# Performance work log

Measured on AMD Instinct MI355X. Metric: run time of the kernel, lower is better.

The kernel has to match this reference:

```python
import jax, jax.numpy as jnp
import numpy as np

N = 200_000          # active voxels
CIN, COUT = 64, 128  # in_filters, out_filters
GRID = (32, 480, 480)  # sparse spatial shape (D, H, W)
NEG_SLOPE = 0.01     # nn.LeakyReLU default
EPS = 1e-5           # BatchNorm1d default


def _build_nbrs():
    """Build rulebook-style neighbor tables for the two submanifold kernels.

    Returns nbr31 [9, N] for kernel (3,1,3) and nbr13 [9, N] for kernel (1,3,3).
    Entry == N means 'no active neighbor' (maps to a zero pad row).
    """
    rng = np.random.default_rng(0)
    prod = GRID[0] * GRID[1] * GRID[2]
    lin = rng.choice(prod, size=N, replace=False)
    z, y, x = np.unravel_index(lin, GRID)
    lut = np.full(prod, N, dtype=np.int64)
    lut[lin] = np.arange(N)

    def nbrs(offsets):
        out = np.full((len(offsets), N), N, dtype=np.int32)
        for k, (dz, dy, dx) in enumerate(offsets):
            zz, yy, xx = z + dz, y + dy, x + dx
            valid = ((zz >= 0) & (zz < GRID[0]) & (yy >= 0) & (yy < GRID[1])
                     & (xx >= 0) & (xx < GRID[2]))
            l2 = (zz * GRID[1] + yy) * GRID[2] + xx
            out[k, valid] = lut[l2[valid]].astype(np.int32)
        return out

    off31 = [(dz, 0, dx) for dz in (-1, 0, 1) for dx in (-1, 0, 1)]  # (3,1,3)
    off13 = [(0, dy, dx) for dy in (-1, 0, 1) for dx in (-1, 0, 1)]  # (1,3,3)
    return nbrs(off31), nbrs(off13)


def setup_inputs() -> dict:
    key = jax.random.key(0)
    ks = jax.random.split(key, 5)
    nbr31, nbr13 = _build_nbrs()
    s_in = (2.0 / (9 * CIN)) ** 0.5
    s_out = (2.0 / (9 * COUT)) ** 0.5
    ones = jnp.ones((COUT,), jnp.float32)
    zeros = jnp.zeros((COUT,), jnp.float32)
    return {
        "feats": jax.random.normal(ks[0], (N, CIN), jnp.float32),
        "W1": jax.random.normal(ks[1], (9, CIN, COUT), jnp.float32) * s_in,
        "W1_2": jax.random.normal(ks[2], (9, COUT, COUT), jnp.float32) * s_out,
        "W2": jax.random.normal(ks[3], (9, CIN, COUT), jnp.float32) * s_in,
        "W3": jax.random.normal(ks[4], (9, COUT, COUT), jnp.float32) * s_out,
        "g0": ones, "b0": zeros,      # bn0  (init: weight=1, bias=0)
        "g0_2": ones, "b0_2": zeros,  # bn0_2
        "g1": ones, "b1": zeros,      # bn1
        "g2": ones, "b2": zeros,      # bn2
        "nbr31": jnp.asarray(nbr31),
        "nbr13": jnp.asarray(nbr13),
    }


def _subm_conv(f, W, nbr):
    # f [N, Cin], W [9, Cin, Cout], nbr [9, N] -> [N, Cout]
    fp = jnp.concatenate([f, jnp.zeros((1, f.shape[1]), f.dtype)], axis=0)
    g = fp[nbr]  # gather: [9, N, Cin]
    return jnp.einsum("knc,kcd->nd", g, W)


def _lrelu(f):
    return jnp.where(f >= 0, f, NEG_SLOPE * f)


def _bn(f, gamma, beta):
    # BatchNorm1d training-mode batch stats (biased variance) over voxel dim
    m = jnp.mean(f, axis=0)
    v = jnp.mean(jnp.square(f), axis=0) - m * m
    return (f - m) * jax.lax.rsqrt(v + EPS) * gamma + beta


def reference(feats, W1, W1_2, W2, W3, g0, b0, g0_2, b0_2, g1, b1, g2, b2,
              nbr31, nbr13):
    shortcut = _bn(_lrelu(_subm_conv(feats, W1, nbr31)), g0, b0)
    shortcut = _bn(_lrelu(_subm_conv(shortcut, W1_2, nbr13)), g0_2, b0_2)
    resA = _bn(_lrelu(_subm_conv(feats, W2, nbr13)), g1, b1)
    resA = _bn(_lrelu(_subm_conv(resA, W3, nbr31)), g2, b2)
    return resA + shortcut
```

## Files before the change

### kernel.cpp

```cpp
#include <hip/hip_runtime.h>

#define NV 200000
#define NCH 391
#define PCAP 56
#define CG 3125
#define PN 3516
#define RB1 110

typedef __attribute__((ext_vector_type(8))) short sh8;
typedef __attribute__((ext_vector_type(4))) float f32x4;
typedef __attribute__((ext_vector_type(2))) unsigned int u32x2;

__device__ inline unsigned short f2bf(float f) {
  unsigned int u = __builtin_bit_cast(unsigned int, f);
  u += 0x7FFFu + ((u >> 16) & 1u);
  return (unsigned short)(u >> 16);
}
__device__ inline float bf2f(unsigned short h) {
  unsigned int u = ((unsigned int)h) << 16;
  return __builtin_bit_cast(float, u);
}
__device__ inline float lrelu(float v) { return v >= 0.f ? v : 0.01f * v; }

__global__ __launch_bounds__(256) void prep_k(
    const float* __restrict__ W1, const float* __restrict__ W12,
    const float* __restrict__ W2, const float* __restrict__ W3,
    unsigned short* __restrict__ T1, unsigned short* __restrict__ T12,
    unsigned short* __restrict__ T2, unsigned short* __restrict__ T3,
    const int* __restrict__ nbr31, const int* __restrict__ nbr13,
    int2* __restrict__ pairs, int* __restrict__ cc) {
  __shared__ unsigned short lt[64 * 130];
  __shared__ int base_s[4];
  __shared__ int run;
  int bx = blockIdx.x;
  const int tid = threadIdx.x;
  if (bx < 36) {
    const float* src;
    unsigned short* dst;
    int cin, k;
    if (bx < 9) { src = W1; dst = T1; cin = 64; k = bx; }
    else if (bx < 18) { src = W2; dst = T2; cin = 64; k = bx - 9; }
    else if (bx < 27) { src = W12; dst = T12; cin = 128; k = bx - 18; }
    else { src = W3; dst = T3; cin = 128; k = bx - 27; }
    src += (size_t)k * cin * 128;
    dst += (size_t)k * 128 * cin;
    const int cmask = cin - 1;
    const int csh = (cin == 64) ? 6 : 7;
    for (int h = 0; h < 2; ++h) {
      if (h) __syncthreads();
      const int tot = cin * 64;
      for (int e = tid; e < tot; e += 256) {
        const int c = e >> 6, dd = e & 63;
        lt[dd * 130 + c] = f2bf(src[c * 128 + h * 64 + dd]);
      }
      __syncthreads();
      for (int o = tid; o < tot; o += 256) {
        const int dl = o >> csh, c = o & cmask;
        dst[(size_t)(h * 64 + dl) * cin + c] = lt[dl * 130 + c];
      }
    }
    return;
  }
  bx -= 36;
  const int slot = bx / NCH, chunk = bx % NCH;
  const int table = slot >> 3, kk = slot & 7;
  const int k = kk + (kk >= 4);
  const int* nb = (table ? nbr13 : nbr31) + (size_t)k * NV;
  const int lane = tid & 63, wv = tid >> 6;
  if (tid == 0) run = 0;
  __syncthreads();
  int2* pw = pairs + (size_t)(slot * NCH + chunk) * PCAP;
#pragma unroll
  for (int i = 0; i < 2; ++i) {
    const int n = chunk * 512 + i * 256 + tid;
    const int val = (n < NV) ? nb[n] : NV;
    const bool valid = (val != NV);
    const unsigned long long m = __ballot(valid);
    const int loff = __popcll(m & ((1ull << lane) - 1ull));
    if (lane == 0) base_s[wv] = __popcll(m);
    __syncthreads();
    int wbase = run;
    for (int w = 0; w < wv; ++w) wbase += base_s[w];
    if (valid) {
      const int pos = wbase + loff;
      if (pos < PCAP) {
        int2 pr;
        pr.x = val;
        pr.y = n;
        pw[pos] = pr;
      }
    }
    __syncthreads();
    if (tid == 0) run += base_s[0] + base_s[1] + base_s[2] + base_s[3];
    __syncthreads();
  }
  if (tid == 0) cc[slot * NCH + chunk] = min(run, PCAP);
}

#define STATS_EMIT(ACC, PART, PROW)                                             \
  {                                                                             \
    f32x4 ssum[2], ssq[2];                                                      \
    _Pragma("unroll") for (int mt = 0; mt < 2; ++mt) {                          \
      ssum[mt] = (f32x4){0.f, 0.f, 0.f, 0.f};                                   \
      ssq[mt] = (f32x4){0.f, 0.f, 0.f, 0.f};                                    \
      _Pragma("unroll") for (int nt = 0; nt < 4; ++nt)                          \
          _Pragma("unroll") for (int q = 0; q < 4; ++q) {                       \
        const float f = lrelu(ACC[mt][nt][q]);                                  \
        ssum[mt][q] += f;                                                       \
        ssq[mt][q] += f * f;                                                    \
      }                                                                         \
      _Pragma("unroll") for (int off = 1; off < 16; off <<= 1)                  \
          _Pragma("unroll") for (int q = 0; q < 4; ++q) {                       \
        ssum[mt][q] += __shfl_xor(ssum[mt][q], off);                            \
        ssq[mt][q] += __shfl_xor(ssq[mt][q], off);                              \
      }                                                                         \
      if (l15 == 0) {                                                           \
        const int d0 = (wv * 2 + mt) * 16 + l4 * 4;                             \
        *(f32x4*)(PART + (size_t)(PROW)*256 + d0) = ssum[mt];                   \
        *(f32x4*)(PART + (size_t)(PROW)*256 + 128 + d0) = ssq[mt];              \
      }                                                                         \
    }                                                                           \
  }

#define TILE_OUT(ACC, YPTR)                                                     \
  {                                                                             \
    __syncthreads();                                                            \
    _Pragma("unroll") for (int mt = 0; mt < 2; ++mt)                            \
        _Pragma("unroll") for (int nt = 0; nt < 4; ++nt) {                      \
      u32x2 pk;                                                                 \
      pk[0] = (unsigned)f2bf(ACC[mt][nt][0]) |                                  \
              ((unsigned)f2bf(ACC[mt][nt][1]) << 16);                           \
      pk[1] = (unsigned)f2bf(ACC[mt][nt][2]) |                                  \
              ((unsigned)f2bf(ACC[mt][nt][3]) << 16);                           \
      *(u32x2*)(&lds[(nt * 16 + l15) * 136 + (wv * 2 + mt) * 16 + l4 * 4]) = pk;\
    }                                                                           \
    __syncthreads();                                                            \
    _Pragma("unroll") for (int j = 0; j < 4; ++j) {                             \
      const int row = j * 16 + (tid >> 4);                                      \
      const int c16 = tid & 15;                                                 \
      const sh8 v = *(const sh8*)(&lds[row * 136 + c16 * 8]);                   \
      *(sh8*)(YPTR + (size_t)(row0 + row) * 128 + c16 * 8) = v;                 \
    }                                                                           \
  }

__global__ __launch_bounds__(256) void center2_k(
    const float* __restrict__ X, const unsigned short* __restrict__ W1t,
    const unsigned short* __restrict__ W2t, unsigned short* __restrict__ Y1,
    unsigned short* __restrict__ Y2, float* __restrict__ PA,
    float* __restrict__ PB) {
  constexpr int CIN = 64, CH = 8;
  __shared__ unsigned short lds[64 * 136];
  const int tid = threadIdx.x, lane = tid & 63, wv = tid >> 6;
  const int l15 = lane & 15, l4 = lane >> 4;
  const int prow = blockIdx.x;
  const int row0 = prow * 64;
  const int js = tid & 7;
#pragma unroll
  for (int i = 0; i < 2; ++i) {
    const int r = (i * 256 + tid) >> 3;
    const f32x4 a = *(const f32x4*)(X + (size_t)(row0 + r) * CIN + js * 8);
    const f32x4 b = *(const f32x4*)(X + (size_t)(row0 + r) * CIN + js * 8 + 4);
    sh8 o;
#pragma unroll
    for (int j = 0; j < 4; ++j) {
      o[j] = (short)f2bf(a[j]);
      o[4 + j] = (short)f2bf(b[j]);
    }
    *(sh8*)(lds + ((size_t)r * CH + (js ^ (r & 7))) * 8) = o;
  }
  __syncthreads();

  f32x4 acc1[2][4], acc2[2][4];
#pragma unroll
  for (int mt = 0; mt < 2; ++mt)
#pragma unroll
    for (int nt = 0; nt < 4; ++nt) {
      acc1[mt][nt] = (f32x4){0.f, 0.f, 0.f, 0.f};
      acc2[mt][nt] = (f32x4){0.f, 0.f, 0.f, 0.f};
    }
  const unsigned short* W1K = W1t + (size_t)(4 * 128) * CIN;
  const unsigned short* W2K = W2t + (size_t)(4 * 128) * CIN;
#pragma unroll
  for (int s = 0; s < 2; ++s) {
    sh8 aw1[2], aw2[2];
#pragma unroll
    for (int mt = 0; mt < 2; ++mt) {
      const int d = (wv * 2 + mt) * 16 + l15;
      aw1[mt] = *(const sh8*)(W1K + (size_t)d * CIN + s * 32 + l4 * 8);
      aw2[mt] = *(const sh8*)(W2K + (size_t)d * CIN + s * 32 + l4 * 8);
    }
#pragma unroll
    for (int nt = 0; nt < 4; ++nt) {
      const int r = nt * 16 + l15;
      const int j = s * 4 + l4;
      const sh8 bx = *(const sh8*)(lds + ((size_t)r * CH + (j ^ (r & 7))) * 8);
#pragma unroll
      for (int mt = 0; mt < 2; ++mt) {
        acc1[mt][nt] =
            __builtin_amdgcn_mfma_f32_16x16x32_bf16(aw1[mt], bx, acc1[mt][nt], 0, 0, 0);
        acc2[mt][nt] =
            __builtin_amdgcn_mfma_f32_16x16x32_bf16(aw2[mt], bx, acc2[mt][nt], 0, 0, 0);
      }
    }
  }
  STATS_EMIT(acc1, PA, prow)
  STATS_EMIT(acc2, PB, prow)
  TILE_OUT(acc1, Y1)
  __syncthreads();
  TILE_OUT(acc2, Y2)
}

__global__ __launch_bounds__(256) void c128m_k(
    const unsigned short* __restrict__ y1, const unsigned short* __restrict__ y2,
    const unsigned short* __restrict__ T12, const unsigned short* __restrict__ T3,
    const float* __restrict__ ab, unsigned short* __restrict__ ysc,
    unsigned short* __restrict__ y3, float* __restrict__ PA,
    float* __restrict__ PB) {
  constexpr int CIN = 128, CH = 16;
  __shared__ unsigned short lds[64 * 136];
  const int bx = blockIdx.x;
  const bool first = bx < CG;
  const unsigned short* X = first ? y1 : y2;
  const unsigned short* Wt = first ? T12 : T3;
  const float* abp = first ? ab : ab + 256;
  unsigned short* Y = first ? ysc : y3;
  float* PART = first ? PA : PB;
  const int prow = first ? bx : bx - CG;
  const int row0 = prow * 64;
  const int tid = threadIdx.x, lane = tid & 63, wv = tid >> 6;
  const int l15 = lane & 15, l4 = lane >> 4;
  const int js = tid & 15;
  const f32x4 aL = *(const f32x4*)(abp + js * 8);
  const f32x4 aH = *(const f32x4*)(abp + js * 8 + 4);
  const f32x4 bL = *(const f32x4*)(abp + 128 + js * 8);
  const f32x4 bH = *(const f32x4*)(abp + 128 + js * 8 + 4);
#pragma unroll
  for (int i = 0; i < 4; ++i) {
    const int r = (i * 256 + tid) >> 4;
    const sh8 v = *(const sh8*)(X + (size_t)(row0 + r) * CIN + js * 8);
    sh8 o;
#pragma unroll
    for (int j = 0; j < 4; ++j) {
      o[j] = (short)f2bf(lrelu(bf2f((unsigned short)v[j])) * aL[j] + bL[j]);
      o[4 + j] = (short)f2bf(lrelu(bf2f((unsigned short)v[4 + j])) * aH[j] + bH[j]);
    }
    *(sh8*)(lds + ((size_t)r * CH + (js ^ (r & 7))) * 8) = o;
  }
  __syncthreads();

  f32x4 acc[2][4];
#pragma unroll
  for (int mt = 0; mt < 2; ++mt)
#pragma unroll
    for (int nt = 0; nt < 4; ++nt) acc[mt][nt] = (f32x4){0.f, 0.f, 0.f, 0.f};

  const unsigned short* WtK = Wt + (size_t)(4 * 128) * CIN;
#pragma unroll
  for (int s = 0; s < 4; ++s) {
    sh8 aw[2];
#pragma unroll
    for (int mt = 0; mt < 2; ++mt) {
      const int d = (wv * 2 + mt) * 16 + l15;
      aw[mt] = *(const sh8*)(WtK + (size_t)d * CIN + s * 32 + l4 * 8);
    }
#pragma unroll
    for (int nt = 0; nt < 4; ++nt) {
      const int r = nt * 16 + l15;
      const int j = s * 4 + l4;
      const sh8 bxv = *(const sh8*)(lds + ((size_t)r * CH + (j ^ (r & 7))) * 8);
#pragma unroll
      for (int mt = 0; mt < 2; ++mt)
        acc[mt][nt] =
            __builtin_amdgcn_mfma_f32_16x16x32_bf16(aw[mt], bxv, acc[mt][nt], 0, 0, 0);
    }
  }
  STATS_EMIT(acc, PART, prow)
  TILE_OUT(acc, Y)
}

__global__ __launch_bounds__(256) void off64_k(
    const float* __restrict__ X, const unsigned short* __restrict__ T1,
    const unsigned short* __restrict__ T2, const int2* __restrict__ pairs,
    const int* __restrict__ cc, unsigned short* __restrict__ y1,
    unsigned short* __restrict__ y2, float* __restrict__ PA,
    float* __restrict__ PB) {
  constexpr int CIN = 64, CH = 8;
  const int layer = blockIdx.x / NCH, chunk = blockIdx.x % NCH;
  const unsigned short* Wt = layer ? T2 : T1;
  unsigned short* Y = layer ? y2 : y1;
  float* PD = layer ? PB : PA;
  const int* ccl = cc + layer * 8 * NCH;
  const int2* pl = pairs + (size_t)layer * 8 * NCH * PCAP;
  __shared__ unsigned short tile[64 * CIN];
  const int tid = threadIdx.x, lane = tid & 63, wv = tid >> 6;
  const int l15 = lane & 15, l4 = lane >> 4;
  const int js = tid & 7;
  f32x4 ds[2], dq[2];
#pragma unroll
  for (int mt = 0; mt < 2; ++mt) {
    ds[mt] = (f32x4){0.f, 0.f, 0.f, 0.f};
    dq[mt] = (f32x4){0.f, 0.f, 0.f, 0.f};
  }

  for (int kk = 0; kk < 8; ++kk) {
    const int n0 = ccl[kk * NCH + chunk];
    if (n0 == 0) continue;
    const int k = kk + (kk >= 4);
    const unsigned short* WtK = Wt + (size_t)k * 128 * CIN;
    const int2* pw = pl + (size_t)(kk * NCH + chunk) * PCAP;
    __syncthreads();
#pragma unroll
    for (int i = 0; i < 2; ++i) {
      const int r = (i * 256 + tid) >> 3;
      const int in = (r < n0) ? pw[r].x : NV;
      sh8 o = (sh8){0, 0, 0, 0, 0, 0, 0, 0};
      if (in != NV) {
        const f32x4 a = *(const f32x4*)(X + (size_t)in * CIN + js * 8);
        const f32x4 b = *(const f32x4*)(X + (size_t)in * CIN + js * 8 + 4);
#pragma unroll
        for (int j = 0; j < 4; ++j) {
          o[j] = (short)f2bf(a[j]);
          o[4 + j] = (short)f2bf(b[j]);
        }
      }
      *(sh8*)(tile + ((size_t)r * CH + (js ^ (r & 7))) * 8) = o;
    }
    __syncthreads();

    f32x4 acc[2][4];
#pragma unroll
    for (int mt = 0; mt < 2; ++mt)
#pragma unroll
      for (int nt = 0; nt < 4; ++nt) acc[mt][nt] = (f32x4){0.f, 0.f, 0.f, 0.f};
#pragma unroll
    for (int s = 0; s < 2; ++s) {
      sh8 aw[2];
#pragma unroll
      for (int mt = 0; mt < 2; ++mt) {
        const int d = (wv * 2 + mt) * 16 + l15;
        aw[mt] = *(const sh8*)(WtK + (size_t)d * CIN + s * 32 + l4 * 8);
      }
#pragma unroll
      for (int nt = 0; nt < 4; ++nt) {
        const int r = nt * 16 + l15;
        const int j = s * 4 + l4;
        const sh8 bxv = *(const sh8*)(tile + ((size_t)r * CH + (j ^ (r & 7))) * 8);
#pragma unroll
        for (int mt = 0; mt < 2; ++mt)
          acc[mt][nt] =
              __builtin_amdgcn_mfma_f32_16x16x32_bf16(aw[mt], bxv, acc[mt][nt], 0, 0, 0);
      }
    }
#pragma unroll
    for (int mt = 0; mt < 2; ++mt)
#pragma unroll
      for (int nt = 0; nt < 4; ++nt) {
        const int rr = nt * 16 + l15;
        const int out = (rr < n0) ? pw[rr].y : NV;
        if (out == NV) continue;
        const int d0 = (wv * 2 + mt) * 16 + l4 * 4;
        unsigned short* p = Y + (size_t)out * 128 + d0;
        const u32x2 old = *(const u32x2*)p;
        u32x2 nw;
        float of[4], sf[4];
        of[0] = bf2f((unsigned short)(old[0] & 0xffff));
        of[1] = bf2f((unsigned short)(old[0] >> 16));
        of[2] = bf2f((unsigned short)(old[1] & 0xffff));
        of[3] = bf2f((unsigned short)(old[1] >> 16));
#pragma unroll
        for (int q = 0; q < 4; ++q) {
          sf[q] = of[q] + acc[mt][nt][q];
          const float ln = lrelu(sf[q]), lo = lrelu(of[q]);
          ds[mt][q] += ln - lo;
          dq[mt][q] += ln * ln - lo * lo;
        }
        nw[0] = (unsigned)f2bf(sf[0]) | ((unsigned)f2bf(sf[1]) << 16);
        nw[1] = (unsigned)f2bf(sf[2]) | ((unsigned)f2bf(sf[3]) << 16);
        *(u32x2*)p = nw;
      }
  }
#pragma unroll
  for (int mt = 0; mt < 2; ++mt) {
#pragma unroll
    for (int off = 1; off < 16; off <<= 1)
#pragma unroll
      for (int q = 0; q < 4; ++q) {
        ds[mt][q] += __shfl_xor(ds[mt][q], off);
        dq[mt][q] += __shfl_xor(dq[mt][q], off);
      }
    if (l15 == 0) {
      const int d0 = (wv * 2 + mt) * 16 + l4 * 4;
      *(f32x4*)(PD + (size_t)(CG + chunk) * 256 + d0) = ds[mt];
      *(f32x4*)(PD + (size_t)(CG + chunk) * 256 + 128 + d0) = dq[mt];
    }
  }
}

__global__ __launch_bounds__(256) void off128m_k(
    const unsigned short* __restrict__ y1, const unsigned short* __restrict__ y2,
    const unsigned short* __restrict__ T12, const unsigned short* __restrict__ T3,
    const int2* __restrict__ pairs, const int* __restrict__ cc,
    const float* __restrict__ ab, unsigned short* __restrict__ ysc,
    unsigned short* __restrict__ y3, float* __restrict__ PA,
    float* __restrict__ PB) {
  constexpr int CIN = 128, CH = 16;
  const int lay = blockIdx.x / NCH, chunk = blockIdx.x % NCH;
  const unsigned short* X = lay ? y2 : y1;
  const unsigned short* Wt = lay ? T3 : T12;
  const float* abp = lay ? ab + 256 : ab;
  unsigned short* Y = lay ? y3 : ysc;
  float* PD = lay ? PB : PA;
  const int2* pt = pairs + (lay ? 0 : (size_t)8 * NCH * PCAP);
  const int* ct = cc + (lay ? 0 : 8 * NCH);
  __shared__ unsigned short tile[64 * CIN];
  const int tid = threadIdx.x, lane = tid & 63, wv = tid >> 6;
  const int l15 = lane & 15, l4 = lane >> 4;
  const int js = tid & 15;
  const f32x4 aL = *(const f32x4*)(abp + js * 8);
  const f32x4 aH = *(const f32x4*)(abp + js * 8 + 4);
  const f32x4 bL = *(const f32x4*)(abp + 128 + js * 8);
  const f32x4 bH = *(const f32x4*)(abp + 128 + js * 8 + 4);
  f32x4 ds[2], dq[2];
#pragma unroll
  for (int mt = 0; mt < 2; ++mt) {
    ds[mt] = (f32x4){0.f, 0.f, 0.f, 0.f};
    dq[mt] = (f32x4){0.f, 0.f, 0.f, 0.f};
  }

  for (int kk = 0; kk < 8; ++kk) {
    const int n0 = ct[kk * NCH + chunk];
    if (n0 == 0) continue;
    const int k = kk + (kk >= 4);
    const unsigned short* WtK = Wt + (size_t)k * 128 * CIN;
    const int2* pw = pt + (size_t)(kk * NCH + chunk) * PCAP;
    __syncthreads();
#pragma unroll
    for (int i = 0; i < 4; ++i) {
      const int r = (i * 256 + tid) >> 4;
      const int in = (r < n0) ? pw[r].x : NV;
      sh8 o = (sh8){0, 0, 0, 0, 0, 0, 0, 0};
      if (in != NV) {
        const sh8 v = *(const sh8*)(X + (size_t)in * CIN + js * 8);
#pragma unroll
        for (int j = 0; j < 4; ++j) {
          o[j] = (short)f2bf(lrelu(bf2f((unsigned short)v[j])) * aL[j] + bL[j]);
          o[4 + j] = (short)f2bf(lrelu(bf2f((unsigned short)v[4 + j])) * aH[j] + bH[j]);
        }
      }
      *(sh8*)(tile + ((size_t)r * CH + (js ^ (r & 7))) * 8) = o;
    }
    __syncthreads();

    f32x4 acc[2][4];
#pragma unroll
    for (int mt = 0; mt < 2; ++mt)
#pragma unroll
      for (int nt = 0; nt < 4; ++nt) acc[mt][nt] = (f32x4){0.f, 0.f, 0.f, 0.f};
#pragma unroll
    for (int s = 0; s < 4; ++s) {
      sh8 aw[2];
#pragma unroll
      for (int mt = 0; mt < 2; ++mt) {
        const int d = (wv * 2 + mt) * 16 + l15;
        aw[mt] = *(const sh8*)(WtK + (size_t)d * CIN + s * 32 + l4 * 8);
      }
#pragma unroll
      for (int nt = 0; nt < 4; ++nt) {
        const int r = nt * 16 + l15;
        const int j = s * 4 + l4;
        const sh8 bxv = *(const sh8*)(tile + ((size_t)r * CH + (j ^ (r & 7))) * 8);
#pragma unroll
        for (int mt = 0; mt < 2; ++mt)
          acc[mt][nt] =
              __builtin_amdgcn_mfma_f32_16x16x32_bf16(aw[mt], bxv, acc[mt][nt], 0, 0, 0);
      }
    }
#pragma unroll
    for (int mt = 0; mt < 2; ++mt)
#pragma unroll
      for (int nt = 0; nt < 4; ++nt) {
        const int rr = nt * 16 + l15;
        const int out = (rr < n0) ? pw[rr].y : NV;
        if (out == NV) continue;
        const int d0 = (wv * 2 + mt) * 16 + l4 * 4;
        unsigned short* p = Y + (size_t)out * 128 + d0;
        const u32x2 old = *(const u32x2*)p;
        u32x2 nw;
        float of[4], sf[4];
        of[0] = bf2f((unsigned short)(old[0] & 0xffff));
        of[1] = bf2f((unsigned short)(old[0] >> 16));
        of[2] = bf2f((unsigned short)(old[1] & 0xffff));
        of[3] = bf2f((unsigned short)(old[1] >> 16));
#pragma unroll
        for (int q = 0; q < 4; ++q) {
          sf[q] = of[q] + acc[mt][nt][q];
          const float ln = lrelu(sf[q]), lo = lrelu(of[q]);
          ds[mt][q] += ln - lo;
          dq[mt][q] += ln * ln - lo * lo;
        }
        nw[0] = (unsigned)f2bf(sf[0]) | ((unsigned)f2bf(sf[1]) << 16);
        nw[1] = (unsigned)f2bf(sf[2]) | ((unsigned)f2bf(sf[3]) << 16);
        *(u32x2*)p = nw;
      }
  }
#pragma unroll
  for (int mt = 0; mt < 2; ++mt) {
#pragma unroll
    for (int off = 1; off < 16; off <<= 1)
#pragma unroll
      for (int q = 0; q < 4; ++q) {
        ds[mt][q] += __shfl_xor(ds[mt][q], off);
        dq[mt][q] += __shfl_xor(dq[mt][q], off);
      }
    if (l15 == 0) {
      const int d0 = (wv * 2 + mt) * 16 + l4 * 4;
      *(f32x4*)(PD + (size_t)(CG + chunk) * 256 + d0) = ds[mt];
      *(f32x4*)(PD + (size_t)(CG + chunk) * 256 + 128 + d0) = dq[mt];
    }
  }
}

__global__ __launch_bounds__(256) void red1_k(const float* __restrict__ PA,
                                              const float* __restrict__ PB,
                                              float* __restrict__ RA,
                                              float* __restrict__ RB) {
  const int tb = blockIdx.x / RB1;
  const int b = blockIdx.x % RB1;
  const float* P = tb ? PB : PA;
  float* R = tb ? RB : RA;
  const int c = threadIdx.x;
  const int r0 = b * 32;
  const int r1 = (r0 + 32 < PN) ? r0 + 32 : PN;
  float s = 0.f;
#pragma unroll 4
  for (int r = r0; r < r1; ++r) s += P[(size_t)r * 256 + c];
  R[(size_t)b * 256 + c] = s;
}

__global__ __launch_bounds__(1024) void fin2_k(
    const float* __restrict__ RA, const float* __restrict__ gA,
    const float* __restrict__ btA, float* __restrict__ abA,
    const float* __restrict__ RB, const float* __restrict__ gB,
    const float* __restrict__ btB, float* __restrict__ abB) {
  const float* R = blockIdx.x ? RB : RA;
  const float* g = blockIdx.x ? gB : gA;
  const float* bt = blockIdx.x ? btB : btA;
  float* abo = blockIdx.x ? abB : abA;
  __shared__ float S[1024];
  const int t = threadIdx.x;
  const int c = t & 255, grp = t >> 8;
  float s = 0.f;
  for (int b = grp; b < RB1; b += 4) s += R[(size_t)b * 256 + c];
  S[t] = s;
  __syncthreads();
  if (t < 256) S[t] = S[t] + S[256 + t] + S[512 + t] + S[768 + t];
  __syncthreads();
  if (t < 128) {
    const float m = S[t] * (1.0f / (float)NV);
    const float v = S[128 + t] * (1.0f / (float)NV) - m * m;
    const float a = g[t] * rsqrtf(v + 1e-5f);
    abo[t] = a;
    abo[128 + t] = bt[t] - m * a;
  }
}

__global__ __launch_bounds__(256) void final_k(const unsigned short* __restrict__ y3,
                                               const unsigned short* __restrict__ ysc,
                                               const float* __restrict__ ab3,
                                               const float* __restrict__ ab1,
                                               float* __restrict__ out) {
  const long i = (long)blockIdx.x * 256 + threadIdx.x;
  if (i >= (long)NV * 16) return;
  const long base = i * 8;
  const int c0 = (int)(base & 127);
  const sh8 v3 = *(const sh8*)(y3 + base);
  const sh8 vs = *(const sh8*)(ysc + base);
  const f32x4 a3L = *(const f32x4*)(ab3 + c0);
  const f32x4 a3H = *(const f32x4*)(ab3 + c0 + 4);
  const f32x4 b3L = *(const f32x4*)(ab3 + 128 + c0);
  const f32x4 b3H = *(const f32x4*)(ab3 + 128 + c0 + 4);
  const f32x4 a1L = *(const f32x4*)(ab1 + c0);
  const f32x4 a1H = *(const f32x4*)(ab1 + c0 + 4);
  const f32x4 b1L = *(const f32x4*)(ab1 + 128 + c0);
  const f32x4 b1H = *(const f32x4*)(ab1 + 128 + c0 + 4);
  f32x4 oL, oH;
#pragma unroll
  for (int j = 0; j < 4; ++j) {
    oL[j] = a3L[j] * lrelu(bf2f((unsigned short)v3[j])) + b3L[j] +
            a1L[j] * lrelu(bf2f((unsigned short)vs[j])) + b1L[j];
    oH[j] = a3H[j] * lrelu(bf2f((unsigned short)v3[4 + j])) + b3H[j] +
            a1H[j] * lrelu(bf2f((unsigned short)vs[4 + j])) + b1H[j];
  }
  *(f32x4*)(out + base) = oL;
  *(f32x4*)(out + base + 4) = oH;
}

extern "C" void kernel_launch(void* const* d_in, const int* in_sizes, int n_in,
                              void* d_out, int out_size, void* d_ws, size_t ws_size,
                              hipStream_t stream) {
  const float* feats = (const float*)d_in[0];
  const float* W1 = (const float*)d_in[1];
  const float* W12 = (const float*)d_in[2];
  const float* W2 = (const float*)d_in[3];
  const float* W3 = (const float*)d_in[4];
  const float* g0 = (const float*)d_in[5];
  const float* b0 = (const float*)d_in[6];
  const float* g02 = (const float*)d_in[7];
  const float* b02 = (const float*)d_in[8];
  const float* g1 = (const float*)d_in[9];
  const float* b1 = (const float*)d_in[10];
  const float* g2 = (const float*)d_in[11];
  const float* b2 = (const float*)d_in[12];
  const int* nbr31 = (const int*)d_in[13];
  const int* nbr13 = (const int*)d_in[14];
  float* out = (float*)d_out;

  char* ws = (char*)d_ws;
  size_t off = 0;
  auto alloc = [&](size_t bytes) {
    char* p = ws + off;
    off = (off + bytes + 255) & ~(size_t)255;
    return p;
  };

  unsigned short* T1 = (unsigned short*)alloc((size_t)9 * 128 * 64 * 2);
  unsigned short* T2 = (unsigned short*)alloc((size_t)9 * 128 * 64 * 2);
  unsigned short* T12 = (unsigned short*)alloc((size_t)9 * 128 * 128 * 2);
  unsigned short* T3 = (unsigned short*)alloc((size_t)9 * 128 * 128 * 2);
  unsigned short* y1 = (unsigned short*)alloc((size_t)NV * 128 * 2);
  unsigned short* y2 = (unsigned short*)alloc((size_t)NV * 128 * 2);
  unsigned short* ysc = (unsigned short*)alloc((size_t)NV * 128 * 2);
  unsigned short* y3 = (unsigned short*)alloc((size_t)NV * 128 * 2);
  float* PA = (float*)alloc((size_t)PN * 256 * 4);
  float* PB = (float*)alloc((size_t)PN * 256 * 4);
  float* RA = (float*)alloc((size_t)RB1 * 256 * 4);
  float* RB = (float*)alloc((size_t)RB1 * 256 * 4);
  float* ab = (float*)alloc(1024 * 4);
  int* cc = (int*)alloc((size_t)16 * NCH * 4);
  int2* pairs = (int2*)alloc((size_t)16 * NCH * PCAP * 8);


  prep_k<<<36 + 16 * NCH, 256, 0, stream>>>(W1, W12, W2, W3, T1, T12, T2, T3,
                                            nbr31, nbr13, pairs, cc);
  center2_k<<<CG, 256, 0, stream>>>(feats, T1, T2, y1, y2, PA, PB);
  off64_k<<<2 * NCH, 256, 0, stream>>>(feats, T1, T2, pairs, cc, y1, y2, PA, PB);
  red1_k<<<2 * RB1, 256, 0, stream>>>(PA, PB, RA, RB);
  fin2_k<<<2, 1024, 0, stream>>>(RA, g0, b0, ab + 0, RB, g1, b1, ab + 256);
  c128m_k<<<2 * CG, 256, 0, stream>>>(y1, y2, T12, T3, ab, ysc, y3, PA, PB);
  off128m_k<<<2 * NCH, 256, 0, stream>>>(y1, y2, T12, T3, pairs, cc, ab, ysc, y3,
                                         PA, PB);
  red1_k<<<2 * RB1, 256, 0, stream>>>(PA, PB, RA, RB);
  fin2_k<<<2, 1024, 0, stream>>>(RA, g02, b02, ab + 512, RB, g2, b2, ab + 768);
  final_k<<<12500, 256, 0, stream>>>(y3, ysc, ab + 768, ab + 512, out);
}
```

Measured before the change: 288.0 us.

## Double-buffer gathered feature tiles across kernel offsets in off64/off128 kernels

Result: slower. 298.7 us (+3.7%).

```diff
diff --git a/kernel.cpp b/kernel.cpp
--- a/kernel.cpp
+++ b/kernel.cpp
@@ -291,10 +291,15 @@
   float* PD = layer ? PB : PA;
   const int* ccl = cc + layer * 8 * NCH;
   const int2* pl = pairs + (size_t)layer * 8 * NCH * PCAP;
-  __shared__ unsigned short tile[64 * CIN];
+  __shared__ unsigned short tile[2][64 * CIN];
   const int tid = threadIdx.x, lane = tid & 63, wv = tid >> 6;
   const int l15 = lane & 15, l4 = lane >> 4;
   const int js = tid & 7;
+  const int sr0 = tid >> 3, sr1 = (256 + tid) >> 3;
+  int n[8];
+#pragma unroll
+  for (int kk = 0; kk < 8; ++kk) n[kk] = ccl[kk * NCH + chunk];
+
   f32x4 ds[2], dq[2];
 #pragma unroll
   for (int mt = 0; mt < 2; ++mt) {
@@ -302,30 +307,44 @@
     dq[mt] = (f32x4){0.f, 0.f, 0.f, 0.f};
   }
 
-  for (int kk = 0; kk < 8; ++kk) {
-    const int n0 = ccl[kk * NCH + chunk];
-    if (n0 == 0) continue;
-    const int k = kk + (kk >= 4);
+  f32x4 ga[2], gb[2];
+  auto gather = [&](int kk) {
+    const int2* pw = pl + (size_t)(kk * NCH + chunk) * PCAP;
+#pragma unroll
+    for (int i = 0; i < 2; ++i) {
+      const int r = i ? sr1 : sr0;
+      const int in = (r < n[kk]) ? pw[r].x : NV;
+      if (in != NV) {
+        ga[i] = *(const f32x4*)(X + (size_t)in * CIN + js * 8);
+        gb[i] = *(const f32x4*)(X + (size_t)in * CIN + js * 8 + 4);
+      } else {
+        ga[i] = (f32x4){0.f, 0.f, 0.f, 0.f};
+        gb[i] = (f32x4){0.f, 0.f, 0.f, 0.f};
+      }
+    }
+  };
+  auto commit = [&](int buf) {
+#pragma unroll
+    for (int i = 0; i < 2; ++i) {
+      const int r = i ? sr1 : sr0;
+      sh8 o;
+#pragma unroll
+      for (int j = 0; j < 4; ++j) {
+        o[j] = (short)f2bf(ga[i][j]);
+        o[4 + j] = (short)f2bf(gb[i][j]);
+      }
+      *(sh8*)(tile[buf] + ((size_t)r * CH + (js ^ (r & 7))) * 8) = o;
+    }
+  };
+
+  gather(0);
+  commit(0);
+  for (int t = 0; t < 8; ++t) {
+    __syncthreads();
+    if (t < 7) gather(t + 1);
+    const int k = t + (t >= 4);
     const unsigned short* WtK = Wt + (size_t)k * 128 * CIN;
-    const int2* pw = pl + (size_t)(kk * NCH + chunk) * PCAP;
-    __syncthreads();
-#pragma unroll
-    for (int i = 0; i < 2; ++i) {
-      const int r = (i * 256 + tid) >> 3;
-      const int in = (r < n0) ? pw[r].x : NV;
-      sh8 o = (sh8){0, 0, 0, 0, 0, 0, 0, 0};
-      if (in != NV) {
-        const f32x4 a = *(const f32x4*)(X + (size_t)in * CIN + js * 8);
-        const f32x4 b = *(const f32x4*)(X + (size_t)in * CIN + js * 8 + 4);
-#pragma unroll
-        for (int j = 0; j < 4; ++j) {
-          o[j] = (short)f2bf(a[j]);
-          o[4 + j] = (short)f2bf(b[j]);
-        }
-      }
-      *(sh8*)(tile + ((size_t)r * CH + (js ^ (r & 7))) * 8) = o;
-    }
-    __syncthreads();
+    const unsigned short* tl = tile[t & 1];
 
     f32x4 acc[2][4];
 #pragma unroll
@@ -344,19 +363,20 @@
       for (int nt = 0; nt < 4; ++nt) {
         const int r = nt * 16 + l15;
         const int j = s * 4 + l4;
-        const sh8 bxv = *(const sh8*)(tile + ((size_t)r * CH + (j ^ (r & 7))) * 8);
+        const sh8 bxv = *(const sh8*)(tl + ((size_t)r * CH + (j ^ (r & 7))) * 8);
 #pragma unroll
         for (int mt = 0; mt < 2; ++mt)
           acc[mt][nt] =
               __builtin_amdgcn_mfma_f32_16x16x32_bf16(aw[mt], bxv, acc[mt][nt], 0, 0, 0);
       }
     }
+    const int2* pw = pl + (size_t)(t * NCH + chunk) * PCAP;
 #pragma unroll
     for (int mt = 0; mt < 2; ++mt)
 #pragma unroll
       for (int nt = 0; nt < 4; ++nt) {
         const int rr = nt * 16 + l15;
-        const int out = (rr < n0) ? pw[rr].y : NV;
+        const int out = (rr < n[t]) ? pw[rr].y : NV;
         if (out == NV) continue;
         const int d0 = (wv * 2 + mt) * 16 + l4 * 4;
         unsigned short* p = Y + (size_t)out * 128 + d0;
@@ -378,6 +398,7 @@
         nw[1] = (unsigned)f2bf(sf[2]) | ((unsigned)f2bf(sf[3]) << 16);
         *(u32x2*)p = nw;
       }
+    if (t < 7) commit((t + 1) & 1);
   }
 #pragma unroll
   for (int mt = 0; mt < 2; ++mt) {
@@ -412,7 +433,7 @@
   float* PD = lay ? PB : PA;
   const int2* pt = pairs + (lay ? 0 : (size_t)8 * NCH * PCAP);
   const int* ct = cc + (lay ? 0 : 8 * NCH);
-  __shared__ unsigned short tile[64 * CIN];
+  __shared__ unsigned short tile[2][64 * CIN];
   const int tid = threadIdx.x, lane = tid & 63, wv = tid >> 6;
   const int l15 = lane & 15, l4 = lane >> 4;
   const int js = tid & 15;
@@ -420,6 +441,10 @@
   const f32x4 aH = *(const f32x4*)(abp + js * 8 + 4);
   const f32x4 bL = *(const f32x4*)(abp + 128 + js * 8);
   const f32x4 bH = *(const f32x4*)(abp + 128 + js * 8 + 4);
+  int n[8];
+#pragma unroll
+  for (int kk = 0; kk < 8; ++kk) n[kk] = ct[kk * NCH + chunk];
+
   f32x4 ds[2], dq[2];
 #pragma unroll
   for (int mt = 0; mt < 2; ++mt) {
@@ -427,29 +452,43 @@
     dq[mt] = (f32x4){0.f, 0.f, 0.f, 0.f};
   }
 
-  for (int kk = 0; kk < 8; ++kk) {
-    const int n0 = ct[kk * NCH + chunk];
-    if (n0 == 0) continue;
-    const int k = kk + (kk >= 4);
-    const unsigned short* WtK = Wt + (size_t)k * 128 * CIN;
+  sh8 gv[4];
+  int gvalid[4];
+  auto gather = [&](int kk) {
     const int2* pw = pt + (size_t)(kk * NCH + chunk) * PCAP;
-    __syncthreads();
 #pragma unroll
     for (int i = 0; i < 4; ++i) {
       const int r = (i * 256 + tid) >> 4;
-      const int in = (r < n0) ? pw[r].x : NV;
+      const int in = (r < n[kk]) ? pw[r].x : NV;
+      gvalid[i] = (in != NV);
+      if (in != NV) gv[i] = *(const sh8*)(X + (size_t)in * CIN + js * 8);
+    }
+  };
+  auto commit = [&](int buf) {
+#pragma unroll
+    for (int i = 0; i < 4; ++i) {
+      const int r = (i * 256 + tid) >> 4;
       sh8 o = (sh8){0, 0, 0, 0, 0, 0, 0, 0};
-      if (in != NV) {
-        const sh8 v = *(const sh8*)(X + (size_t)in * CIN + js * 8);
+      if (gvalid[i]) {
 #pragma unroll
         for (int j = 0; j < 4; ++j) {
-          o[j] = (short)f2bf(lrelu(bf2f((unsigned short)v[j])) * aL[j] + bL[j]);
-          o[4 + j] = (short)f2bf(lrelu(bf2f((unsigned short)v[4 + j])) * aH[j] + bH[j]);
+          o[j] = (short)f2bf(lrelu(bf2f((unsigned short)gv[i][j])) * aL[j] + bL[j]);
+          o[4 + j] =
+              (short)f2bf(lrelu(bf2f((unsigned short)gv[i][4 + j])) * aH[j] + bH[j]);
         }
       }
-      *(sh8*)(tile + ((size_t)r * CH + (js ^ (r & 7))) * 8) = o;
-    }
+      *(sh8*)(tile[buf] + ((size_t)r * CH + (js ^ (r & 7))) * 8) = o;
+    }
+  };
+
+  gather(0);
+  commit(0);
+  for (int t = 0; t < 8; ++t) {
     __syncthreads();
+    if (t < 7) gather(t + 1);
+    const int k = t + (t >= 4);
+    const unsigned short* WtK = Wt + (size_t)k * 128 * CIN;
+    const unsigned short* tl = tile[t & 1];
 
     f32x4 acc[2][4];
 #pragma unroll
@@ -468,19 +507,20 @@
       for (int nt = 0; nt < 4; ++nt) {
         const int r = nt * 16 + l15;
         const int j = s * 4 + l4;
-        const sh8 bxv = *(const sh8*)(tile + ((size_t)r * CH + (j ^ (r & 7))) * 8);
+        const sh8 bxv = *(const sh8*)(tl + ((size_t)r * CH + (j ^ (r & 7))) * 8);
 #pragma unroll
         for (int mt = 0; mt < 2; ++mt)
           acc[mt][nt] =
               __builtin_amdgcn_mfma_f32_16x16x32_bf16(aw[mt], bxv, acc[mt][nt], 0, 0, 0);
       }
     }
+    const int2* pw = pt + (size_t)(t * NCH + chunk) * PCAP;
 #pragma unroll
     for (int mt = 0; mt < 2; ++mt)
 #pragma unroll
       for (int nt = 0; nt < 4; ++nt) {
         const int rr = nt * 16 + l15;
-        const int out = (rr < n0) ? pw[rr].y : NV;
+        const int out = (rr < n[t]) ? pw[rr].y : NV;
         if (out == NV) continue;
         const int d0 = (wv * 2 + mt) * 16 + l4 * 4;
         unsigned short* p = Y + (size_t)out * 128 + d0;
@@ -502,6 +542,7 @@
         nw[1] = (unsigned)f2bf(sf[2]) | ((unsigned)f2bf(sf[3]) << 16);
         *(u32x2*)p = nw;
       }
+    if (t < 7) commit((t + 1) & 1);
   }
 #pragma unroll
   for (int mt = 0; mt < 2; ++mt) {
```
